# Performance work log

Measured on AMD Instinct MI355X. Metric: run time of the kernel, lower is better.

The kernel has to match this reference:

```python
import jax, jax.numpy as jnp
import numpy as np

N = 50000       # nodes_num
DIN = 256       # input_dim
DOUT = 128      # output_dim
C = 2           # class_size
HOP = 2
DEV = 3         # device_num
E = 500_000     # edges per device view
M = 10_000      # masked train nodes


def setup_inputs() -> dict:
    key = jax.random.key(0)
    ks = jax.random.split(key, 13)
    return {
        "x": jax.random.normal(ks[0], (N, DIN), jnp.float32),
        "label": jax.random.normal(ks[1], (N, C), jnp.float32),
        "idx_mask": jax.random.randint(ks[2], (M,), 0, N, jnp.int32),
        "src": jax.random.randint(ks[3], (DEV, E), 0, N, jnp.int32),
        "dst": jax.random.randint(ks[4], (DEV, E), 0, N, jnp.int32),
        "vals": jax.random.uniform(ks[5], (DEV, E), jnp.float32),
        "h0": jax.random.normal(ks[6], (N, DOUT), jnp.float32) * 0.05,
        "Ws": jax.random.normal(ks[7], (HOP, DIN, DOUT), jnp.float32) * (6.0 / (DIN + DOUT)) ** 0.5,
        "Vs": jax.random.normal(ks[8], (HOP, DOUT, DOUT), jnp.float32) * (6.0 / (2 * DOUT)) ** 0.5,
        "alphas": jax.random.normal(ks[9], (HOP, DEV), jnp.float32) * 0.5,
        "Wc": jax.random.normal(ks[10], (DOUT, C), jnp.float32) * (6.0 / (DOUT + C)) ** 0.5,
        "b": jnp.zeros((1, C), jnp.float32),
        "u": jax.random.normal(ks[11], (1, DOUT), jnp.float32) * 0.1,
    }


def _gem_layer(x, h, src, dst, vals, W, V, alpha):
    # h1 = x @ W  : dense projection of raw features
    h1 = x @ W  # [N, DOUT]
    # per-device sparse aggregation: (A_d @ h) @ V, alpha-weighted combine
    h2 = jnp.zeros_like(h1)
    for d in range(src.shape[0]):  # small fixed device count
        msgs = vals[d][:, None] * h[src[d]]                       # [E, DOUT] gather
        agg = jax.ops.segment_sum(msgs, dst[d], num_segments=h.shape[0])  # [N, DOUT] scatter-add
        h2 = h2 + alpha[d] * (agg @ V)
    return jax.nn.sigmoid(h1 + h2)


def reference(x, label, idx_mask, src, dst, vals, h0, Ws, Vs, alphas, Wc, b, u):
    h = h0
    for i in range(Ws.shape[0]):  # hop loop, fresh GEMLayer params each hop
        h = _gem_layer(x, h, src, dst, vals, Ws[i], Vs[i], alphas[i])
    masked_data = h[idx_mask]       # [M, DOUT]
    masked_label = label[idx_mask]  # [M, C]
    # eq.(7): -sum log sigmoid(y * u h^T), broadcast [M,C]*[M,1]
    score = masked_data @ u[0]      # [M]
    loss = -jnp.sum(jax.nn.log_sigmoid(masked_label * score[:, None]))
    logits = masked_data @ Wc + b   # [M, C]
    acc = jnp.mean((jnp.argmax(logits, axis=1) == jnp.argmax(masked_label, axis=1)).astype(jnp.float32))
    return loss, acc
```

## Files before the change

### kernel.cpp

```cpp
#include <hip/hip_runtime.h>
#include <hip/hip_bf16.h>

#define N_NODES 50000
#define DIN     256
#define DOUT    128
#define NCLS    2
#define NHOP    2
#define NDEV    3
#define EDG     500000
#define TE      (NDEV*EDG)
#define NMASK   10000
#define LOSS_BLOCKS 2500

#define BUCK    128
#define NBUCK   391
#define CH      2048
#define NBLKA   733
#define BHN     (NBUCK*NBLKA)
#define SCT     512
#define SCANBLKS ((BHN + SCT - 1) / SCT)

typedef __attribute__((ext_vector_type(8))) short bf16x8;
typedef __attribute__((ext_vector_type(4))) float f32x4;
typedef __attribute__((ext_vector_type(2))) float f32x2;

__device__ __forceinline__ float softplusf(float a) {
    return fmaxf(a, 0.f) + log1pf(expf(-fabsf(a)));
}

__device__ __forceinline__ f32x2 fp8lo(unsigned g) {
    return __builtin_amdgcn_cvt_pk_f32_fp8(g, false);
}
__device__ __forceinline__ f32x2 fp8hi(unsigned g) {
    return __builtin_amdgcn_cvt_pk_f32_fp8(g, true);
}
__device__ __forceinline__ unsigned char fp8enc1(float v) {
    return (unsigned char)(__builtin_amdgcn_cvt_pk_fp8_f32(v, v, 0, false) & 0xFF);
}


__global__ __launch_bounds__(256) void k_bhist(const int* __restrict__ dst,
                                               int* __restrict__ bh) {
    __shared__ int hist[NBUCK];
    int blk = blockIdx.x, tid = threadIdx.x;
    for (int i = tid; i < NBUCK; i += 256) hist[i] = 0;
    __syncthreads();
    int base = blk * CH;
    int lim = min(base + CH, TE);
    for (int i = base + tid; i < lim; i += 256) atomicAdd(&hist[dst[i] >> 7], 1);
    __syncthreads();
    for (int i = tid; i < NBUCK; i += 256) bh[(size_t)i * NBLKA + blk] = hist[i];
}

__global__ __launch_bounds__(SCT) void k_scanA(const int* __restrict__ in,
                                               int* __restrict__ out,
                                               int* __restrict__ bsums, int n) {
    __shared__ int s[SCT];
    int tid = threadIdx.x, gid = blockIdx.x * SCT + tid;
    int v = (gid < n) ? in[gid] : 0;
    s[tid] = v; __syncthreads();
    for (int o = 1; o < SCT; o <<= 1) {
        int t = (tid >= o) ? s[tid - o] : 0;
        __syncthreads();
        s[tid] += t;
        __syncthreads();
    }
    if (gid < n) out[gid] = s[tid] - v;
    if (tid == SCT - 1) bsums[blockIdx.x] = s[SCT - 1];
}

__global__ __launch_bounds__(SCT) void k_scanB(int* __restrict__ bsums, int nb) {
    __shared__ int s[SCT];
    int tid = threadIdx.x;
    int carry = 0;
    for (int base = 0; base < nb; base += SCT) {
        int v = (base + tid < nb) ? bsums[base + tid] : 0;
        s[tid] = v; __syncthreads();
        for (int o = 1; o < SCT; o <<= 1) {
            int t = (tid >= o) ? s[tid - o] : 0;
            __syncthreads();
            s[tid] += t;
            __syncthreads();
        }
        if (base + tid < nb) bsums[base + tid] = s[tid] - v + carry;
        carry += s[SCT - 1];
        __syncthreads();
    }
}

__global__ __launch_bounds__(SCT) void k_scanC(int* __restrict__ out,
                                               const int* __restrict__ bsums, int n) {
    int gid = blockIdx.x * SCT + threadIdx.x;
    if (gid < n) out[gid] += bsums[blockIdx.x];
}

__global__ __launch_bounds__(256) void k_bbin(const int* __restrict__ src,
                                              const int* __restrict__ dst,
                                              const float* __restrict__ vals,
                                              const int* __restrict__ sc,
                                              uint2* __restrict__ ebkt) {
    __shared__ int cur[NBUCK];
    int blk = blockIdx.x, tid = threadIdx.x;
    for (int i = tid; i < NBUCK; i += 256) cur[i] = sc[(size_t)i * NBLKA + blk];
    __syncthreads();
    int base = blk * CH;
    int lim = min(base + CH, TE);
    for (int i = base + tid; i < lim; i += 256) {
        int d = i / EDG;
        int n = dst[i];
        int bu = n >> 7;
        int pos = atomicAdd(&cur[bu], 1);
        ebkt[pos] = make_uint2((unsigned)src[i] | ((unsigned)d << 16) |
                               ((unsigned)(n & 127) << 18),
                               __float_as_uint(vals[i]));
    }
}

__global__ __launch_bounds__(256) void k_bsort(const uint2* __restrict__ ebkt,
                                               const int* __restrict__ sc,
                                               const float* __restrict__ alphas,
                                               uint2* __restrict__ edh0,
                                               uint2* __restrict__ edh1,
                                               int* __restrict__ offs) {
    __shared__ int cnt[BUCK], start[BUCK + 1], cur[BUCK];
    int b = blockIdx.x, tid = threadIdx.x;
    float a00 = alphas[0], a01 = alphas[1], a02 = alphas[2];
    float a10 = alphas[3], a11 = alphas[4], a12 = alphas[5];
    int beg = sc[(size_t)b * NBLKA];
    int end = (b + 1 < NBUCK) ? sc[(size_t)(b + 1) * NBLKA] : TE;
    if (tid < BUCK) { cnt[tid] = 0; cur[tid] = 0; }
    __syncthreads();
    for (int e = beg + tid; e < end; e += 256)
        atomicAdd(&cnt[(ebkt[e].x >> 18) & 127], 1);
    __syncthreads();
    if (tid == 0) {
        int acc = 0;
        for (int i = 0; i < BUCK; ++i) { start[i] = acc; acc += cnt[i]; }
        start[BUCK] = acc;
    }
    __syncthreads();
    if (tid < BUCK) {
        int n = b * BUCK + tid;
        if (n < N_NODES) offs[n] = beg + start[tid];
    }
    if (b == 0 && tid == 255) offs[N_NODES] = TE;
    for (int e = beg + tid; e < end; e += 256) {
        uint2 v = ebkt[e];
        int dl = (v.x >> 18) & 127;
        int pos = beg + start[dl] + atomicAdd(&cur[dl], 1);
        unsigned s = v.x & 0xFFFFu;
        int d = (v.x >> 16) & 3;
        float val = __uint_as_float(v.y);
        float w0 = val * (d == 0 ? a00 : (d == 1 ? a01 : a02));
        float w1 = val * (d == 0 ? a10 : (d == 1 ? a11 : a12));
        edh0[pos] = make_uint2(s, __float_as_uint(w0));
        edh1[pos] = make_uint2(s, __float_as_uint(w1));
    }
}

__global__ void k_cvt(const float* __restrict__ in, __hip_bfloat16* __restrict__ out, int n2) {
    int i = blockIdx.x * blockDim.x + threadIdx.x;
    if (i >= n2) return;
    float2 f = ((const float2*)in)[i];
    __hip_bfloat162 b;
    b.x = __float2bfloat16(f.x);
    b.y = __float2bfloat16(f.y);
    ((__hip_bfloat162*)out)[i] = b;
}

__global__ void k_cvt8(const float* __restrict__ in, unsigned char* __restrict__ out, int n4) {
    int i = blockIdx.x * blockDim.x + threadIdx.x;
    if (i >= n4) return;
    float4 f = ((const float4*)in)[i];
    int r = 0;
    r = __builtin_amdgcn_cvt_pk_fp8_f32(f.x, f.y, r, false);
    r = __builtin_amdgcn_cvt_pk_fp8_f32(f.z, f.w, r, true);
    ((unsigned*)out)[i] = (unsigned)r;
}

__global__ void k_tw(const float* __restrict__ Ws, const float* __restrict__ Vs,
                     __hip_bfloat16* __restrict__ WsT, __hip_bfloat16* __restrict__ VsT) {
    int i = blockIdx.x * 256 + threadIdx.x;
    if (i < NHOP * DIN * DOUT) {
        int hop = i / (DIN * DOUT);
        int r = i % (DIN * DOUT);
        int k = r >> 7, n = r & 127;
        WsT[(size_t)hop * DOUT * DIN + (size_t)n * DIN + k] = __float2bfloat16(Ws[i]);
    } else {
        int j = i - NHOP * DIN * DOUT;
        if (j < NHOP * DOUT * DOUT) {
            int hop = j / (DOUT * DOUT);
            int r = j % (DOUT * DOUT);
            int k = r >> 7, n = r & 127;
            VsT[(size_t)hop * DOUT * DOUT + (size_t)n * DOUT + k] = __float2bfloat16(Vs[j]);
        }
    }
}

__global__ __launch_bounds__(256) void k_agg(const unsigned char* __restrict__ h8,
                                             const uint2* __restrict__ edh,
                                             const int* __restrict__ offs,
                                             __hip_bfloat16* __restrict__ aggcb) {
    int wid = threadIdx.x >> 6;
    int lane = threadIdx.x & 63;
    int n = blockIdx.x * 4 + wid;
    if (n >= N_NODES) return;
    int grp = lane >> 3;
    int cw = lane & 7;
    int beg = offs[n], end = offs[n + 1];
    float a[16];
#pragma unroll
    for (int j = 0; j < 16; ++j) a[j] = 0.f;

    for (int e = beg; e < end; e += 8) {
        int rem = end - e;
        int ee = e + (grp < rem ? grp : 0);
        uint2 q = edh[ee];
        float wt = (grp < rem) ? __uint_as_float(q.y) : 0.f;
        uint4 g = *(const uint4*)(h8 + (size_t)q.x * DOUT + cw * 16);
#pragma unroll
        for (int wv = 0; wv < 4; ++wv) {
            unsigned gw = (&g.x)[wv];
            f32x2 lo = fp8lo(gw), hi = fp8hi(gw);
            a[wv * 4 + 0] += wt * lo[0];
            a[wv * 4 + 1] += wt * lo[1];
            a[wv * 4 + 2] += wt * hi[0];
            a[wv * 4 + 3] += wt * hi[1];
        }
    }
#pragma unroll
    for (int j = 0; j < 16; ++j) {
        a[j] += __shfl_xor(a[j], 8, 64);
        a[j] += __shfl_xor(a[j], 16, 64);
        a[j] += __shfl_xor(a[j], 32, 64);
    }
    if (grp == 0) {
        union { __hip_bfloat16 h[8]; uint4 u; } pk0, pk1;
#pragma unroll
        for (int j = 0; j < 8; ++j) {
            pk0.h[j] = __float2bfloat16(a[j]);
            pk1.h[j] = __float2bfloat16(a[8 + j]);
        }
        *(uint4*)(aggcb + (size_t)n * DOUT + cw * 16) = pk0.u;
        *(uint4*)(aggcb + (size_t)n * DOUT + cw * 16 + 8) = pk1.u;
    }
}

__global__ __launch_bounds__(256) void k_mm(const __hip_bfloat16* __restrict__ A1,
                                            const __hip_bfloat16* __restrict__ BT1,
                                            const __hip_bfloat16* __restrict__ A2,
                                            const __hip_bfloat16* __restrict__ BT2,
                                            unsigned char* __restrict__ C8,
                                            __hip_bfloat16* __restrict__ Cbf,
                                            int M, int K1, int K2) {
    __shared__ short As[128][40];
    __shared__ short Bs[128][40];
    int tid = threadIdx.x;
    int lane = tid & 63;
    int w = tid >> 6;
    int wr = (w >> 1) * 64, wc = (w & 1) * 64;
    int lr = lane & 15, kg = lane >> 4;
    int row0 = blockIdx.x * 128;

    f32x4 acc[4][4];
#pragma unroll
    for (int mi = 0; mi < 4; ++mi)
#pragma unroll
        for (int ni = 0; ni < 4; ++ni) acc[mi][ni] = (f32x4){0.f, 0.f, 0.f, 0.f};

#pragma unroll
    for (int seg = 0; seg < 2; ++seg) {
        const __hip_bfloat16* A = seg ? A2 : A1;
        const __hip_bfloat16* BT = seg ? BT2 : BT1;
        int K = seg ? K2 : K1;
        for (int k0 = 0; k0 < K; k0 += 32) {
#pragma unroll
            for (int j = 0; j < 2; ++j) {
                int c = tid + j * 256;
                int r = c >> 2, kc = (c & 3) * 8;
                bf16x8 g = {};
                int gr = row0 + r;
                if (gr < M) g = *(const bf16x8*)(A + (size_t)gr * K + k0 + kc);
                *(bf16x8*)&As[r][kc] = g;
            }
#pragma unroll
            for (int j = 0; j < 2; ++j) {
                int c = tid + j * 256;
                int r = c >> 2, kc = (c & 3) * 8;
                *(bf16x8*)&Bs[r][kc] = *(const bf16x8*)(BT + (size_t)r * K + k0 + kc);
            }
            __syncthreads();
            bf16x8 af[4], bfr[4];
#pragma unroll
            for (int i = 0; i < 4; ++i) {
                af[i]  = *(const bf16x8*)&As[wr + i * 16 + lr][kg * 8];
                bfr[i] = *(const bf16x8*)&Bs[wc + i * 16 + lr][kg * 8];
            }
#pragma unroll
            for (int mi = 0; mi < 4; ++mi)
#pragma unroll
                for (int ni = 0; ni < 4; ++ni)
                    acc[mi][ni] = __builtin_amdgcn_mfma_f32_16x16x32_bf16(
                        af[mi], bfr[ni], acc[mi][ni], 0, 0, 0);
            __syncthreads();
        }
    }

#pragma unroll
    for (int mi = 0; mi < 4; ++mi) {
#pragma unroll
        for (int r = 0; r < 4; ++r) {
            int row = row0 + wr + mi * 16 + kg * 4 + r;
            if (row < M) {
#pragma unroll
                for (int ni = 0; ni < 4; ++ni) {
                    int col = wc + ni * 16 + lr;
                    float v = acc[mi][ni][r];
                    v = 1.f / (1.f + __expf(-v));
                    if (C8)  C8[(size_t)row * DOUT + col] = fp8enc1(v);
                    if (Cbf) Cbf[(size_t)row * DOUT + col] = __float2bfloat16(v);
                }
            }
        }
    }
}

__global__ __launch_bounds__(256) void k_loss(const __hip_bfloat16* __restrict__ h,
                                              const float* __restrict__ label,
                                              const int* __restrict__ idx,
                                              const float* __restrict__ u,
                                              const float* __restrict__ Wc,
                                              const float* __restrict__ bb,
                                              float* __restrict__ blockpart, int Mtot) {
    __shared__ float sl[4], sc2[4];
    int wid = threadIdx.x >> 6;
    int lane = threadIdx.x & 63;
    int w = blockIdx.x * 4 + wid;
    float lsum = 0.f, csum = 0.f;
    if (w < Mtot) {
        int node = idx[w];
        float v0 = __bfloat162float(h[(size_t)node * DOUT + lane]);
        float v1 = __bfloat162float(h[(size_t)node * DOUT + 64 + lane]);
        float ps = v0 * u[lane] + v1 * u[64 + lane];
        float p0 = v0 * Wc[lane * 2 + 0] + v1 * Wc[(lane + 64) * 2 + 0];
        float p1 = v0 * Wc[lane * 2 + 1] + v1 * Wc[(lane + 64) * 2 + 1];
#pragma unroll
        for (int o = 32; o > 0; o >>= 1) {
            ps += __shfl_xor(ps, o, 64);
            p0 += __shfl_xor(p0, o, 64);
            p1 += __shfl_xor(p1, o, 64);
        }
        if (lane == 0) {
            float y0 = label[(size_t)node * NCLS + 0];
            float y1 = label[(size_t)node * NCLS + 1];
            lsum = softplusf(-(y0 * ps)) + softplusf(-(y1 * ps));
            float l0 = p0 + bb[0], l1 = p1 + bb[1];
            int pred = (l1 > l0) ? 1 : 0;
            int truth = (y1 > y0) ? 1 : 0;
            csum = (pred == truth) ? 1.f : 0.f;
        }
    }
    if (lane == 0) { sl[wid] = lsum; sc2[wid] = csum; }
    __syncthreads();
    if (threadIdx.x == 0) {
        blockpart[blockIdx.x * 2 + 0] = sl[0] + sl[1] + sl[2] + sl[3];
        blockpart[blockIdx.x * 2 + 1] = sc2[0] + sc2[1] + sc2[2] + sc2[3];
    }
}

__global__ __launch_bounds__(256) void k_final(const float* __restrict__ bp,
                                               float* __restrict__ out, int nb) {
    __shared__ float sl[256], sc2[256];
    int t = threadIdx.x;
    float l = 0.f, c = 0.f;
    for (int i = t; i < nb; i += 256) { l += bp[i * 2]; c += bp[i * 2 + 1]; }
    sl[t] = l; sc2[t] = c;
    __syncthreads();
    for (int o = 128; o > 0; o >>= 1) {
        if (t < o) { sl[t] += sl[t + o]; sc2[t] += sc2[t + o]; }
        __syncthreads();
    }
    if (t == 0) { out[0] = sl[0]; out[1] = sc2[0] * (1.0f / NMASK); }
}

extern "C" void kernel_launch(void* const* d_in, const int* in_sizes, int n_in,
                              void* d_out, int out_size, void* d_ws, size_t ws_size,
                              hipStream_t stream) {
    const float* x      = (const float*)d_in[0];
    const float* label  = (const float*)d_in[1];
    const int*   idx    = (const int*)d_in[2];
    const int*   src    = (const int*)d_in[3];
    const int*   dst    = (const int*)d_in[4];
    const float* vals   = (const float*)d_in[5];
    const float* h0     = (const float*)d_in[6];
    const float* Ws     = (const float*)d_in[7];
    const float* Vs     = (const float*)d_in[8];
    const float* alphas = (const float*)d_in[9];
    const float* Wc     = (const float*)d_in[10];
    const float* bb     = (const float*)d_in[11];
    const float* u      = (const float*)d_in[12];
    float* out = (float*)d_out;

    char* p = (char*)d_ws;
    __hip_bfloat16* aggcb = (__hip_bfloat16*)p; p += (size_t)N_NODES * DOUT * 2;
    __hip_bfloat16* xb    = (__hip_bfloat16*)p; p += (size_t)N_NODES * DIN * 2;
    unsigned char*  h8    = (unsigned char*)p;  p += (size_t)N_NODES * DOUT;
    uint2*          edh0  = (uint2*)p;          p += (size_t)TE * 8;
    uint2*          edh1  = (uint2*)p;          p += (size_t)TE * 8;
    int*            offs  = (int*)p;            p += 200064 * 4;
    __hip_bfloat16* WsT   = (__hip_bfloat16*)p; p += (size_t)NHOP * DOUT * DIN * 2;
    __hip_bfloat16* VsT   = (__hip_bfloat16*)p; p += (size_t)NHOP * DOUT * DOUT * 2;
    float*          blockpart = (float*)p;      p += LOSS_BLOCKS * 2 * 4;
    uint2* ebkt  = (uint2*)xb;
    int*   bh    = (int*)((char*)xb + (size_t)TE * 8);
    int*   sc    = bh + BHN;
    int*   bsums = sc + BHN;
    __hip_bfloat16* hbf = (__hip_bfloat16*)edh1;

    k_bhist<<<NBLKA, 256, 0, stream>>>(dst, bh);
    k_scanA<<<SCANBLKS, SCT, 0, stream>>>(bh, sc, bsums, BHN);
    k_scanB<<<1, SCT, 0, stream>>>(bsums, SCANBLKS);
    k_scanC<<<SCANBLKS, SCT, 0, stream>>>(sc, bsums, BHN);
    k_bbin<<<NBLKA, 256, 0, stream>>>(src, dst, vals, sc, ebkt);
    k_bsort<<<NBUCK, 256, 0, stream>>>(ebkt, sc, alphas, edh0, edh1, offs);

    k_cvt8<<<(N_NODES * DOUT / 4 + 255) / 256, 256, 0, stream>>>(h0, h8, N_NODES * DOUT / 4);
    k_cvt<<<(N_NODES * DIN / 2 + 255) / 256, 256, 0, stream>>>(x, xb, N_NODES * DIN / 2);
    k_tw<<<(NHOP * (DIN * DOUT + DOUT * DOUT) + 255) / 256, 256, 0, stream>>>(Ws, Vs, WsT, VsT);

    const int MMBLK = (N_NODES + 127) / 128;
    k_agg<<<(N_NODES + 3) / 4, 256, 0, stream>>>(h8, edh0, offs, aggcb);
    k_mm<<<MMBLK, 256, 0, stream>>>(xb, WsT, aggcb, VsT, h8, nullptr, N_NODES, DIN, DOUT);
    k_agg<<<(N_NODES + 3) / 4, 256, 0, stream>>>(h8, edh1, offs, aggcb);
    k_mm<<<MMBLK, 256, 0, stream>>>(xb, WsT + (size_t)DOUT * DIN, aggcb,
                                    VsT + (size_t)DOUT * DOUT, nullptr, hbf,
                                    N_NODES, DIN, DOUT);

    k_loss<<<LOSS_BLOCKS, 256, 0, stream>>>(hbf, label, idx, u, Wc, bb, blockpart, NMASK);
    k_final<<<1, 256, 0, stream>>>(blockpart, out, LOSS_BLOCKS);
}
```

Before: 207.0 us.

## Fuse sparse aggregation and dual GEMM into one per-hop kernel

```diff
diff --git a/kernel.cpp b/kernel.cpp
--- a/kernel.cpp
+++ b/kernel.cpp
@@ -197,70 +197,66 @@
     }
 }
 
-__global__ __launch_bounds__(256) void k_agg(const unsigned char* __restrict__ h8,
-                                             const uint2* __restrict__ edh,
-                                             const int* __restrict__ offs,
-                                             __hip_bfloat16* __restrict__ aggcb) {
-    int wid = threadIdx.x >> 6;
-    int lane = threadIdx.x & 63;
-    int n = blockIdx.x * 4 + wid;
-    if (n >= N_NODES) return;
-    int grp = lane >> 3;
-    int cw = lane & 7;
-    int beg = offs[n], end = offs[n + 1];
-    float a[16];
-#pragma unroll
-    for (int j = 0; j < 16; ++j) a[j] = 0.f;
-
-    for (int e = beg; e < end; e += 8) {
-        int rem = end - e;
-        int ee = e + (grp < rem ? grp : 0);
-        uint2 q = edh[ee];
-        float wt = (grp < rem) ? __uint_as_float(q.y) : 0.f;
-        uint4 g = *(const uint4*)(h8 + (size_t)q.x * DOUT + cw * 16);
-#pragma unroll
-        for (int wv = 0; wv < 4; ++wv) {
-            unsigned gw = (&g.x)[wv];
-            f32x2 lo = fp8lo(gw), hi = fp8hi(gw);
-            a[wv * 4 + 0] += wt * lo[0];
-            a[wv * 4 + 1] += wt * lo[1];
-            a[wv * 4 + 2] += wt * hi[0];
-            a[wv * 4 + 3] += wt * hi[1];
-        }
-    }
-#pragma unroll
-    for (int j = 0; j < 16; ++j) {
-        a[j] += __shfl_xor(a[j], 8, 64);
-        a[j] += __shfl_xor(a[j], 16, 64);
-        a[j] += __shfl_xor(a[j], 32, 64);
-    }
-    if (grp == 0) {
-        union { __hip_bfloat16 h[8]; uint4 u; } pk0, pk1;
-#pragma unroll
-        for (int j = 0; j < 8; ++j) {
-            pk0.h[j] = __float2bfloat16(a[j]);
-            pk1.h[j] = __float2bfloat16(a[8 + j]);
-        }
-        *(uint4*)(aggcb + (size_t)n * DOUT + cw * 16) = pk0.u;
-        *(uint4*)(aggcb + (size_t)n * DOUT + cw * 16 + 8) = pk1.u;
-    }
-}
-
-__global__ __launch_bounds__(256) void k_mm(const __hip_bfloat16* __restrict__ A1,
-                                            const __hip_bfloat16* __restrict__ BT1,
-                                            const __hip_bfloat16* __restrict__ A2,
-                                            const __hip_bfloat16* __restrict__ BT2,
-                                            unsigned char* __restrict__ C8,
-                                            __hip_bfloat16* __restrict__ Cbf,
-                                            int M, int K1, int K2) {
-    __shared__ short As[128][40];
-    __shared__ short Bs[128][40];
+__global__ __launch_bounds__(256, 4) void k_hop(const unsigned char* __restrict__ h8in,
+                                                const __hip_bfloat16* __restrict__ xb,
+                                                const __hip_bfloat16* __restrict__ WT,
+                                                const __hip_bfloat16* __restrict__ VT,
+                                                const uint2* __restrict__ edh,
+                                                const int* __restrict__ offs,
+                                                unsigned char* __restrict__ C8,
+                                                __hip_bfloat16* __restrict__ Cbf) {
+    __shared__ short aggL[128][136];
     int tid = threadIdx.x;
     int lane = tid & 63;
-    int w = tid >> 6;
-    int wr = (w >> 1) * 64, wc = (w & 1) * 64;
+    int wid = tid >> 6;
+    int row0 = blockIdx.x * 128;
+    int grp = lane >> 3, cw = lane & 7;
+
+    for (int nl = wid * 32; nl < wid * 32 + 32; ++nl) {
+        int node = row0 + nl;
+        float a[16];
+#pragma unroll
+        for (int j = 0; j < 16; ++j) a[j] = 0.f;
+        if (node < N_NODES) {
+            int beg = offs[node], end = offs[node + 1];
+            for (int e = beg; e < end; e += 8) {
+                int rem = end - e;
+                int ee = e + (grp < rem ? grp : 0);
+                uint2 q = edh[ee];
+                float wt = (grp < rem) ? __uint_as_float(q.y) : 0.f;
+                uint4 g = *(const uint4*)(h8in + (size_t)q.x * DOUT + cw * 16);
+#pragma unroll
+                for (int wv = 0; wv < 4; ++wv) {
+                    unsigned gw = (&g.x)[wv];
+                    f32x2 lo = fp8lo(gw), hi = fp8hi(gw);
+                    a[wv * 4 + 0] += wt * lo[0];
+                    a[wv * 4 + 1] += wt * lo[1];
+                    a[wv * 4 + 2] += wt * hi[0];
+                    a[wv * 4 + 3] += wt * hi[1];
+                }
+            }
+        }
+#pragma unroll
+        for (int j = 0; j < 16; ++j) {
+            a[j] += __shfl_xor(a[j], 8, 64);
+            a[j] += __shfl_xor(a[j], 16, 64);
+            a[j] += __shfl_xor(a[j], 32, 64);
+        }
+        if (grp == 0) {
+            union { __hip_bfloat16 h[8]; uint4 u; } pk0, pk1;
+#pragma unroll
+            for (int j = 0; j < 8; ++j) {
+                pk0.h[j] = __float2bfloat16(a[j]);
+                pk1.h[j] = __float2bfloat16(a[8 + j]);
+            }
+            *(uint4*)&aggL[nl][cw * 16] = pk0.u;
+            *(uint4*)&aggL[nl][cw * 16 + 8] = pk1.u;
+        }
+    }
+    __syncthreads();
+
+    int wr = (wid >> 1) * 64, wc = (wid & 1) * 64;
     int lr = lane & 15, kg = lane >> 4;
-    int row0 = blockIdx.x * 128;
 
     f32x4 acc[4][4];
 #pragma unroll
@@ -268,42 +264,33 @@
 #pragma unroll
         for (int ni = 0; ni < 4; ++ni) acc[mi][ni] = (f32x4){0.f, 0.f, 0.f, 0.f};
 
-#pragma unroll
-    for (int seg = 0; seg < 2; ++seg) {
-        const __hip_bfloat16* A = seg ? A2 : A1;
-        const __hip_bfloat16* BT = seg ? BT2 : BT1;
-        int K = seg ? K2 : K1;
-        for (int k0 = 0; k0 < K; k0 += 32) {
-#pragma unroll
-            for (int j = 0; j < 2; ++j) {
-                int c = tid + j * 256;
-                int r = c >> 2, kc = (c & 3) * 8;
-                bf16x8 g = {};
-                int gr = row0 + r;
-                if (gr < M) g = *(const bf16x8*)(A + (size_t)gr * K + k0 + kc);
-                *(bf16x8*)&As[r][kc] = g;
-            }
-#pragma unroll
-            for (int j = 0; j < 2; ++j) {
-                int c = tid + j * 256;
-                int r = c >> 2, kc = (c & 3) * 8;
-                *(bf16x8*)&Bs[r][kc] = *(const bf16x8*)(BT + (size_t)r * K + k0 + kc);
-            }
-            __syncthreads();
-            bf16x8 af[4], bfr[4];
-#pragma unroll
-            for (int i = 0; i < 4; ++i) {
-                af[i]  = *(const bf16x8*)&As[wr + i * 16 + lr][kg * 8];
-                bfr[i] = *(const bf16x8*)&Bs[wc + i * 16 + lr][kg * 8];
-            }
-#pragma unroll
-            for (int mi = 0; mi < 4; ++mi)
-#pragma unroll
-                for (int ni = 0; ni < 4; ++ni)
-                    acc[mi][ni] = __builtin_amdgcn_mfma_f32_16x16x32_bf16(
-                        af[mi], bfr[ni], acc[mi][ni], 0, 0, 0);
-            __syncthreads();
-        }
+    for (int k0 = 0; k0 < DIN; k0 += 32) {
+        bf16x8 af[4], bfr[4];
+#pragma unroll
+        for (int i = 0; i < 4; ++i) {
+            af[i]  = *(const bf16x8*)(xb + (size_t)(row0 + wr + i * 16 + lr) * DIN + k0 + kg * 8);
+            bfr[i] = *(const bf16x8*)(WT + (size_t)(wc + i * 16 + lr) * DIN + k0 + kg * 8);
+        }
+#pragma unroll
+        for (int mi = 0; mi < 4; ++mi)
+#pragma unroll
+            for (int ni = 0; ni < 4; ++ni)
+                acc[mi][ni] = __builtin_amdgcn_mfma_f32_16x16x32_bf16(
+                    af[mi], bfr[ni], acc[mi][ni], 0, 0, 0);
+    }
+    for (int k0 = 0; k0 < DOUT; k0 += 32) {
+        bf16x8 af[4], bfr[4];
+#pragma unroll
+        for (int i = 0; i < 4; ++i) {
+            af[i]  = *(const bf16x8*)&aggL[wr + i * 16 + lr][k0 + kg * 8];
+            bfr[i] = *(const bf16x8*)(VT + (size_t)(wc + i * 16 + lr) * DOUT + k0 + kg * 8);
+        }
+#pragma unroll
+        for (int mi = 0; mi < 4; ++mi)
+#pragma unroll
+            for (int ni = 0; ni < 4; ++ni)
+                acc[mi][ni] = __builtin_amdgcn_mfma_f32_16x16x32_bf16(
+                    af[mi], bfr[ni], acc[mi][ni], 0, 0, 0);
     }
 
 #pragma unroll
@@ -311,7 +298,7 @@
 #pragma unroll
         for (int r = 0; r < 4; ++r) {
             int row = row0 + wr + mi * 16 + kg * 4 + r;
-            if (row < M) {
+            if (row < N_NODES) {
 #pragma unroll
                 for (int ni = 0; ni < 4; ++ni) {
                     int col = wc + ni * 16 + lr;
@@ -402,9 +389,10 @@
     float* out = (float*)d_out;
 
     char* p = (char*)d_ws;
-    __hip_bfloat16* aggcb = (__hip_bfloat16*)p; p += (size_t)N_NODES * DOUT * 2;
     __hip_bfloat16* xb    = (__hip_bfloat16*)p; p += (size_t)N_NODES * DIN * 2;
-    unsigned char*  h8    = (unsigned char*)p;  p += (size_t)N_NODES * DOUT;
+    unsigned char*  h8a   = (unsigned char*)p;  p += (size_t)N_NODES * DOUT;
+    unsigned char*  h8b   = (unsigned char*)p;  p += (size_t)N_NODES * DOUT;
+    __hip_bfloat16* hbf   = (__hip_bfloat16*)p; p += (size_t)N_NODES * DOUT * 2;
     uint2*          edh0  = (uint2*)p;          p += (size_t)TE * 8;
     uint2*          edh1  = (uint2*)p;          p += (size_t)TE * 8;
     int*            offs  = (int*)p;            p += 200064 * 4;
@@ -415,7 +403,6 @@
     int*   bh    = (int*)((char*)xb + (size_t)TE * 8);
     int*   sc    = bh + BHN;
     int*   bsums = sc + BHN;
-    __hip_bfloat16* hbf = (__hip_bfloat16*)edh1;
 
     k_bhist<<<NBLKA, 256, 0, stream>>>(dst, bh);
     k_scanA<<<SCANBLKS, SCT, 0, stream>>>(bh, sc, bsums, BHN);
@@ -424,17 +411,14 @@
     k_bbin<<<NBLKA, 256, 0, stream>>>(src, dst, vals, sc, ebkt);
     k_bsort<<<NBUCK, 256, 0, stream>>>(ebkt, sc, alphas, edh0, edh1, offs);
 
-    k_cvt8<<<(N_NODES * DOUT / 4 + 255) / 256, 256, 0, stream>>>(h0, h8, N_NODES * DOUT / 4);
+    k_cvt8<<<(N_NODES * DOUT / 4 + 255) / 256, 256, 0, stream>>>(h0, h8a, N_NODES * DOUT / 4);
     k_cvt<<<(N_NODES * DIN / 2 + 255) / 256, 256, 0, stream>>>(x, xb, N_NODES * DIN / 2);
     k_tw<<<(NHOP * (DIN * DOUT + DOUT * DOUT) + 255) / 256, 256, 0, stream>>>(Ws, Vs, WsT, VsT);
 
-    const int MMBLK = (N_NODES + 127) / 128;
-    k_agg<<<(N_NODES + 3) / 4, 256, 0, stream>>>(h8, edh0, offs, aggcb);
-    k_mm<<<MMBLK, 256, 0, stream>>>(xb, WsT, aggcb, VsT, h8, nullptr, N_NODES, DIN, DOUT);
-    k_agg<<<(N_NODES + 3) / 4, 256, 0, stream>>>(h8, edh1, offs, aggcb);
-    k_mm<<<MMBLK, 256, 0, stream>>>(xb, WsT + (size_t)DOUT * DIN, aggcb,
-                                    VsT + (size_t)DOUT * DOUT, nullptr, hbf,
-                                    N_NODES, DIN, DOUT);
+    k_hop<<<NBUCK, 256, 0, stream>>>(h8a, xb, WsT, VsT, edh0, offs, h8b, nullptr);
+    k_hop<<<NBUCK, 256, 0, stream>>>(h8b, xb, WsT + (size_t)DOUT * DIN,
+                                     VsT + (size_t)DOUT * DOUT, edh1, offs,
+                                     nullptr, hbf);
 
     k_loss<<<LOSS_BLOCKS, 256, 0, stream>>>(hbf, label, idx, u, Wc, bb, blockpart, NMASK);
     k_final<<<1, 256, 0, stream>>>(blockpart, out, LOSS_BLOCKS);
```

Result: slower. 368.1 us (+77.8%).
